# Optimization experiments

Hardware: AMD Instinct MI355X
Metric: run time of the kernel (lower is better)

## Reference

```python
import jax, jax.numpy as jnp
import numpy as np

B, N_REL, N_OBJ, N_ATT, VOCAB, D = 32, 1024, 1024, 4, 2048, 512


def setup_inputs() -> dict:
    key = jax.random.key(0)
    ks = jax.random.split(key, 12)
    inp = {}
    inp["ssg_rel"] = jax.random.randint(ks[0], (B, N_REL, 3), 0, N_OBJ, dtype=jnp.int32)
    inp["ssg_obj"] = jax.random.randint(ks[1], (B, N_OBJ), 0, VOCAB, dtype=jnp.int32)
    inp["ssg_att"] = jax.random.randint(ks[2], (B, N_OBJ, N_ATT), 0, VOCAB, dtype=jnp.int32)
    inp["emb_table"] = jax.random.normal(ks[3], (VOCAB, D), jnp.float32) * 0.02
    def lin(k, fan_in):
        return jax.random.normal(k, (fan_in, D), jnp.float32) * (1.0 / np.sqrt(fan_in))
    inp["W_sbj"] = lin(ks[4], 3 * D); inp["b_sbj"] = jnp.zeros((D,), jnp.float32)
    inp["W_obj"] = lin(ks[5], 3 * D); inp["b_obj"] = jnp.zeros((D,), jnp.float32)
    inp["W_rel"] = lin(ks[6], 3 * D); inp["b_rel"] = jnp.zeros((D,), jnp.float32)
    inp["W_o"] = lin(ks[7], D);      inp["b_o"] = jnp.zeros((D,), jnp.float32)
    inp["W_a"] = lin(ks[8], 2 * D);  inp["b_a"] = jnp.zeros((D,), jnp.float32)
    return inp


def reference(ssg_rel, ssg_obj, ssg_att, emb_table,
              W_sbj, b_sbj, W_obj, b_obj, W_rel, b_rel, W_o, b_o, W_a, b_a):
    # Dropout is identity in eval mode.
    Bq, N_rel, _ = ssg_rel.shape
    _, N_obj, N_att = ssg_att.shape
    d = emb_table.shape[1]

    rel_mask = (ssg_rel[:, :, 2] == 1)[..., None]      # [B, N_rel, 1], True = pad
    obj_mask = ssg_obj == 1                            # [B, N_obj]
    attr_mask = ssg_att == 1                           # [B, N_obj, N_att]

    rel_emb = emb_table[ssg_rel[:, :, 2]]              # [B, N_rel, d]
    obj_emb = emb_table[ssg_obj]                       # [B, N_obj, d]
    attr_emb = emb_table[ssg_att]                      # [B, N_obj, N_att, d]

    sbj_id = ssg_rel[:, :, 0]
    obj_id = ssg_rel[:, :, 1]
    gather = lambda ids: jnp.take_along_axis(obj_emb, ids[..., None], axis=1)  # [B,N_rel,d]
    sbj_g = gather(sbj_id)
    obj_g = gather(obj_id)

    zfill = lambda x: jnp.where(rel_mask, 0.0, x)
    # Sequential overwriting matches the original: rel_obj/rel_rel use the UPDATED sbj/obj feats.
    sbj_f = zfill(jax.nn.relu(jnp.concatenate([sbj_g, obj_g, rel_emb], -1) @ W_sbj + b_sbj))
    obj_f = zfill(jax.nn.relu(jnp.concatenate([sbj_f, obj_g, rel_emb], -1) @ W_obj + b_obj))
    rel_f = zfill(jax.nn.relu(jnp.concatenate([sbj_f, obj_f, rel_emb], -1) @ W_rel + b_rel))

    node = jnp.where(obj_mask[..., None], 0.0, jax.nn.relu(obj_emb @ W_o + b_o))  # [B,N_obj,d]

    att_in = jnp.concatenate(
        [jnp.broadcast_to(obj_emb[:, :, None, :], (Bq, N_obj, N_att, d)), attr_emb], -1)
    att_f = jnp.where(attr_mask[..., None], 0.0, jax.nn.relu(att_in @ W_a + b_a))  # [B,N_obj,N_att,d]

    bidx = jnp.arange(Bq)[:, None]
    node = node.at[bidx, sbj_id].add(sbj_f)
    node = node.at[bidx, obj_id].add(obj_f)

    # Original builds counts=ones(B, 2*N_rel, N_obj+1) then scatters 1s into it -> a no-op,
    # so counts.sum(dim=1) == 2*N_rel everywhere; the divisor is the constant 2*N_rel.
    rel_object_feat = node / jnp.asarray(2.0 * N_rel, node.dtype)

    att_sum = att_f.sum(axis=2)                        # [B, N_obj, d]
    att_cnt = jnp.sum(~attr_mask, axis=-1)             # [B, N_obj] number of valid attrs
    attr_zero = att_cnt == 0
    denom = jnp.maximum(att_cnt, 1).astype(att_sum.dtype)[..., None]
    att_feat = jnp.where(attr_zero[..., None], 0.0, att_sum / denom)

    ssg_feat = jnp.concatenate([rel_object_feat, rel_f, att_feat], axis=1)
    ssg_mask = jnp.concatenate([obj_mask, rel_mask[..., 0], attr_zero], axis=1)[:, None, None, :]
    return ssg_feat, ssg_mask
```

## Files before the change

kernel.cpp:

```cpp
#include <hip/hip_runtime.h>
#include <hip/hip_bf16.h>

typedef __attribute__((ext_vector_type(8))) short bf16x8;
typedef __attribute__((ext_vector_type(4))) float f32x4;

#define N_OBJ 1024
#define N_REL 1024
#define NB 32
#define D 512
#define VOCAB 2048
#define M_ROWS (NB * N_REL)
#define PRE_BLK (VOCAB * D)
#define WT_BLK (D * D)
#define LCAP 64

__device__ __forceinline__ ushort f2bf(float f) {
    union { float f; unsigned u; } v; v.f = f;
    unsigned u = v.u;
    unsigned r = (u + 0x7FFFu + ((u >> 16) & 1u)) >> 16;
    return (ushort)r;
}
__device__ __forceinline__ float bf2f(ushort h) {
    union { unsigned u; float f; } v; v.u = ((unsigned)h) << 16;
    return v.f;
}

__device__ __forceinline__ void gload16(const ushort* g, const ushort* l) {
    __builtin_amdgcn_global_load_lds(
        (const __attribute__((address_space(1))) void*)(unsigned long long)(const void*)g,
        (__attribute__((address_space(3))) void*)(unsigned)(unsigned long long)(const void*)l,
        16, 0, 0);
}
__device__ __forceinline__ unsigned lds_off(const void* p) {
    return (unsigned)(unsigned long long)(const __attribute__((address_space(3))) void*)p;
}
__device__ __forceinline__ bf16x8 ds_read128(unsigned off) {
    bf16x8 r;
    asm volatile("ds_read_b128 %0, %1" : "=v"(r) : "v"(off));
    return r;
}

template <int MODE>
__device__ __forceinline__ void gemm8_body(
    int mt, int nt, int q, int tid, ushort* lds,
    const ushort* __restrict__ A, const ushort* __restrict__ WT,
    ushort* __restrict__ PREB,
    const int* __restrict__ ssg_rel, const int* __restrict__ ssg_obj,
    const float* __restrict__ bias,
    ushort* __restrict__ featbuf, float* __restrict__ out0,
    float* __restrict__ out1) {
    constexpr int KTOT = (MODE == 2) ? 1024 : 512;
    constexpr int NK = KTOT / 32;
    constexpr int LDA = (MODE == 0) ? 512 : 1024;

    const int m0 = mt * 256, n0 = nt * 256;

    const ushort* BT0;
    const ushort* BT1 = nullptr;
    ushort* PREq = nullptr;
    if (MODE == 0) {
        const int wtq[9] = {0, 1, 2, 4, 5, 8, 9, 10, 11};
        BT0 = WT + (size_t)wtq[q] * WT_BLK + (size_t)n0 * 512;
        PREq = PREB + (size_t)q * PRE_BLK;
    } else if (MODE == 1) {
        BT0 = WT + (size_t)3 * WT_BLK + (size_t)n0 * 512;
    } else {
        BT0 = WT + (size_t)6 * WT_BLK + (size_t)n0 * 512;
        BT1 = WT + (size_t)7 * WT_BLK + (size_t)n0 * 512;
    }

    const ushort* Ag = A + (size_t)m0 * LDA;
    const int srow = tid >> 2;
    const int scol = (tid & 3) * 8;

    const int wave = tid >> 6, lane = tid & 63;
    const int wm = wave >> 2, wn = wave & 3;
    const int lr = lane & 15, lk = lane >> 4;

    f32x4 acc[8][4];
#pragma unroll
    for (int mi = 0; mi < 8; mi++)
#pragma unroll
        for (int ni = 0; ni < 4; ni++)
            acc[mi][ni] = (f32x4){0.f, 0.f, 0.f, 0.f};

#define STAGE(KT) do {                                                          \
        int _b = (KT) & 3;                                                      \
        ushort* _dA = &lds[(_b * 2 + 0) * 8192];                                \
        ushort* _dB = &lds[(_b * 2 + 1) * 8192];                                \
        int _k0 = (KT) * 32;                                                    \
        const ushort* _Bb = (MODE == 2 && _k0 >= 512) ? (BT1 + (_k0 - 512))     \
                                                      : (BT0 + _k0);            \
        gload16(Ag + (size_t)(srow) * LDA + _k0 + scol, _dA + srow * 32 + scol);        \
        gload16(Ag + (size_t)(srow + 128) * LDA + _k0 + scol, _dA + (srow + 128) * 32 + scol); \
        gload16(_Bb + (size_t)(srow) * 512 + scol, _dB + srow * 32 + scol);             \
        gload16(_Bb + (size_t)(srow + 128) * 512 + scol, _dB + (srow + 128) * 32 + scol); \
    } while (0)

    STAGE(0); STAGE(1); STAGE(2);

    for (int kt = 0; kt < NK; ++kt) {
        if (kt + 3 < NK) {
            asm volatile("s_waitcnt vmcnt(8)\n\ts_barrier" ::: "memory");
            STAGE(kt + 3);
        } else if (kt + 3 == NK) {
            asm volatile("s_waitcnt vmcnt(8)\n\ts_barrier" ::: "memory");
        } else if (kt + 2 == NK) {
            asm volatile("s_waitcnt vmcnt(4)\n\ts_barrier" ::: "memory");
        } else {
            asm volatile("s_waitcnt vmcnt(0)\n\ts_barrier" ::: "memory");
        }
        {
            int buf = kt & 3;
            unsigned baseA = lds_off(&lds[(buf * 2 + 0) * 8192]) + (unsigned)(wm * 128) * 64 + lk * 16;
            unsigned baseB = lds_off(&lds[(buf * 2 + 1) * 8192]) + (unsigned)(wn * 64) * 64 + lk * 16;
            bf16x8 bfr[4], af[8];
#pragma unroll
            for (int ni = 0; ni < 4; ni++)
                bfr[ni] = ds_read128(baseB + (unsigned)(ni * 16 + lr) * 64);
#pragma unroll
            for (int mi = 0; mi < 8; mi++)
                af[mi] = ds_read128(baseA + (unsigned)(mi * 16 + lr) * 64);
            asm volatile("s_waitcnt lgkmcnt(4)" ::: "memory");
            __builtin_amdgcn_sched_barrier(0);
            __builtin_amdgcn_s_setprio(1);
#pragma unroll
            for (int mi = 0; mi < 4; mi++)
#pragma unroll
                for (int ni = 0; ni < 4; ni++)
                    acc[mi][ni] = __builtin_amdgcn_mfma_f32_16x16x32_bf16(af[mi], bfr[ni], acc[mi][ni], 0, 0, 0);
            __builtin_amdgcn_s_setprio(0);
            asm volatile("s_waitcnt lgkmcnt(0)" ::: "memory");
            __builtin_amdgcn_sched_barrier(0);
            __builtin_amdgcn_s_setprio(1);
#pragma unroll
            for (int mi = 4; mi < 8; mi++)
#pragma unroll
                for (int ni = 0; ni < 4; ni++)
                    acc[mi][ni] = __builtin_amdgcn_mfma_f32_16x16x32_bf16(af[mi], bfr[ni], acc[mi][ni], 0, 0, 0);
            __builtin_amdgcn_s_setprio(0);
        }
    }
#undef STAGE

    if (MODE == 0) {
#pragma unroll
        for (int mi = 0; mi < 8; mi++)
#pragma unroll
            for (int ni = 0; ni < 4; ni++) {
                int ch = n0 + wn * 64 + ni * 16 + lr;
#pragma unroll
                for (int j = 0; j < 4; j++) {
                    int R = m0 + wm * 128 + mi * 16 + lk * 4 + j;
                    PREq[(size_t)R * 512 + ch] = f2bf(acc[mi][ni][j]);
                }
            }
        return;
    }

    __syncthreads();
    int* sIo  = (int*)lds;
    int* sRid = sIo + 256;
    if (tid < 256) {
        int R = m0 + tid;
        int rid = ssg_rel[R * 3 + 2];
        sRid[tid] = rid;
        if (MODE == 1) sIo[tid] = ssg_obj[(R & ~(N_OBJ - 1)) + ssg_rel[R * 3 + 1]];
        if (MODE == 2 && nt == 0) {
            int b = R >> 10, rr = R & (N_REL - 1);
            out1[(size_t)b * 3072 + 1024 + rr] = (rid == 1) ? 1.0f : 0.0f;
        }
    }
    __syncthreads();

#pragma unroll
    for (int mi = 0; mi < 8; mi++) {
#pragma unroll
        for (int ni = 0; ni < 4; ni++) {
            int ch = n0 + wn * 64 + ni * 16 + lr;
#pragma unroll
            for (int j = 0; j < 4; j++) {
                int rl = wm * 128 + mi * 16 + lk * 4 + j;
                int R = m0 + rl;
                float v = acc[mi][ni][j];
                if (MODE == 1) {
                    int rid = sRid[rl];
                    int io = sIo[rl];
                    float t = v + bf2f(PREB[(size_t)3 * PRE_BLK + (size_t)io * 512 + ch])
                                + bf2f(PREB[(size_t)4 * PRE_BLK + (size_t)rid * 512 + ch])
                                + bias[ch];
                    t = fmaxf(t, 0.f);
                    if (rid == 1) t = 0.f;
                    featbuf[(size_t)R * 1024 + 512 + ch] = f2bf(t);
                } else {
                    int rid = sRid[rl];
                    float t = v + bf2f(PREB[(size_t)5 * PRE_BLK + (size_t)rid * 512 + ch])
                                + bias[ch];
                    t = fmaxf(t, 0.f);
                    if (rid == 1) t = 0.f;
                    int b = R >> 10, rr = R & (N_REL - 1);
                    out0[((size_t)(b * 3072 + 1024 + rr)) * 512 + ch] = t;
                }
            }
        }
    }
}

__global__ __launch_bounds__(256)
void k_setup(const float* __restrict__ E, ushort* __restrict__ EB,
             const float* __restrict__ Wsbj, const float* __restrict__ Wobj,
             const float* __restrict__ Wrel, const float* __restrict__ Wo,
             const float* __restrict__ Wa, ushort* __restrict__ WT,
             int* __restrict__ cnt) {
    int blk = blockIdx.x, tid = threadIdx.x;
    if (blk < 1024) {
        int i = blk * 256 + tid;
        float4 v = ((const float4*)E)[i];
        ushort4 o; o.x = f2bf(v.x); o.y = f2bf(v.y); o.z = f2bf(v.z); o.w = f2bf(v.w);
        ((ushort4*)EB)[i] = o;
    } else if (blk < 4096) {
        __shared__ float s[32][33];
        int bb = blk - 1024;
        int q = bb >> 8, rem = bb & 255;
        int bx = rem & 15, by = rem >> 4;
        const float* src; int ro;
        if (q < 3)       { src = Wsbj; ro = q * 512; }
        else if (q < 6)  { src = Wobj; ro = (q - 3) * 512; }
        else if (q < 9)  { src = Wrel; ro = (q - 6) * 512; }
        else if (q == 9) { src = Wo;   ro = 0; }
        else             { src = Wa;   ro = (q - 10) * 512; }
        int tx = tid & 31, ty = tid >> 5;
        int kbase = by * 32, nbase = bx * 32;
#pragma unroll
        for (int i = 0; i < 4; i++) {
            int k = kbase + ty + i * 8;
            s[ty + i * 8][tx] = src[(size_t)(ro + k) * 512 + nbase + tx];
        }
        __syncthreads();
        ushort* dst = WT + (size_t)q * WT_BLK;
#pragma unroll
        for (int i = 0; i < 4; i++) {
            int n = nbase + ty + i * 8;
            dst[(size_t)n * 512 + kbase + tx] = f2bf(s[tx][ty + i * 8]);
        }
    } else {
        cnt[(blk - 4096) * 256 + tid] = 0;
    }
}

__global__ __launch_bounds__(512, 2)
void k_pre_fill(const ushort* __restrict__ EB, const ushort* __restrict__ WT,
                ushort* __restrict__ PREB, const int* __restrict__ ssg_rel,
                int* __restrict__ cnt, int* __restrict__ lists) {
    __shared__ __attribute__((aligned(16))) ushort lds[4 * 2 * 256 * 32];
    int blk = blockIdx.x, tid = threadIdx.x;
    if (blk < 120) {
        int q, mt, nt;
        if (blk < 96) {
            const int qf[6] = {0, 1, 3, 6, 7, 8};
            q = qf[blk >> 4]; mt = (blk & 15) >> 1; nt = blk & 1;
        } else {
            const int qh[3] = {2, 4, 5};
            int b = blk - 96;
            q = qh[b >> 3]; mt = (b & 7) >> 1; nt = b & 1;
        }
        gemm8_body<0>(mt, nt, q, tid, lds, EB, WT, PREB,
                      nullptr, nullptr, nullptr, nullptr, nullptr, nullptr);
    } else {
        int r = (blk - 120) * 512 + tid;
        int bb = r & ~(N_OBJ - 1);
        int sid = ssg_rel[r * 3 + 0];
        int oid = ssg_rel[r * 3 + 1];
        int s0 = atomicAdd(&cnt[bb + sid], 1);
        if (s0 < LCAP) lists[(size_t)(bb + sid) * LCAP + s0] = r * 2;
        int s1 = atomicAdd(&cnt[bb + oid], 1);
        if (s1 < LCAP) lists[(size_t)(bb + oid) * LCAP + s1] = r * 2 + 1;
    }
}

__global__ void k_sbj_att(const int* __restrict__ ssg_rel, const int* __restrict__ ssg_obj,
                          const int* __restrict__ ssg_att,
                          const ushort* __restrict__ PREB,
                          const float* __restrict__ b_sbj, const float* __restrict__ b_a,
                          ushort* __restrict__ featbuf,
                          float* __restrict__ out0, float* __restrict__ out1) {
    int blk = blockIdx.x, tid = threadIdx.x;
    if (blk < 16384) {
        int R = blk * 2 + (tid >> 7);
        int c4 = tid & 127;
        int sid = ssg_rel[R * 3 + 0];
        int oid = ssg_rel[R * 3 + 1];
        int rid = ssg_rel[R * 3 + 2];
        int bb = R & ~(N_OBJ - 1);
        int is_ = ssg_obj[bb + sid];
        int io  = ssg_obj[bb + oid];
        ushort4 p1 = ((const ushort4*)(PREB + (size_t)is_ * 512))[c4];
        ushort4 p2 = ((const ushort4*)(PREB + (size_t)1 * PRE_BLK + (size_t)io * 512))[c4];
        ushort4 p3 = ((const ushort4*)(PREB + (size_t)2 * PRE_BLK + (size_t)rid * 512))[c4];
        float4 b  = ((const float4*)b_sbj)[c4];
        float4 v;
        v.x = fmaxf(bf2f(p1.x) + bf2f(p2.x) + bf2f(p3.x) + b.x, 0.f);
        v.y = fmaxf(bf2f(p1.y) + bf2f(p2.y) + bf2f(p3.y) + b.y, 0.f);
        v.z = fmaxf(bf2f(p1.z) + bf2f(p2.z) + bf2f(p3.z) + b.z, 0.f);
        v.w = fmaxf(bf2f(p1.w) + bf2f(p2.w) + bf2f(p3.w) + b.w, 0.f);
        if (rid == 1) { v.x = v.y = v.z = v.w = 0.f; }
        ushort4 o; o.x = f2bf(v.x); o.y = f2bf(v.y); o.z = f2bf(v.z); o.w = f2bf(v.w);
        *(ushort4*)&featbuf[(size_t)R * 1024 + c4 * 4] = o;
    } else {
        int Ro = (blk - 16384) * 2 + (tid >> 7);
        int c4 = tid & 127;
        int iv = ssg_obj[Ro];
        int bq = Ro >> 10, o = Ro & (N_OBJ - 1);
        int4 jj = ((const int4*)ssg_att)[Ro];
        int j0 = jj.x, j1 = jj.y, j2 = jj.z, j3 = jj.w;
        float4 ba4 = ((const float4*)b_a)[c4];
        ushort4 q7 = ((const ushort4*)(PREB + (size_t)7 * PRE_BLK + (size_t)iv * 512))[c4];
        float bx = bf2f(q7.x) + ba4.x, by = bf2f(q7.y) + ba4.y;
        float bz = bf2f(q7.z) + ba4.z, bw = bf2f(q7.w) + ba4.w;
        int cnt = (j0 != 1) + (j1 != 1) + (j2 != 1) + (j3 != 1);
        float inv = cnt ? 1.0f / (float)cnt : 0.f;
        float sx = 0.f, sy = 0.f, sz = 0.f, sw = 0.f;
        const ushort* A2 = PREB + (size_t)8 * PRE_BLK;
#define ACC_ATT(J) if ((J) != 1) { \
            ushort4 a2 = ((const ushort4*)(A2 + (size_t)(J) * 512))[c4]; \
            sx += fmaxf(bx + bf2f(a2.x), 0.f); sy += fmaxf(by + bf2f(a2.y), 0.f); \
            sz += fmaxf(bz + bf2f(a2.z), 0.f); sw += fmaxf(bw + bf2f(a2.w), 0.f); }
        ACC_ATT(j0) ACC_ATT(j1) ACC_ATT(j2) ACC_ATT(j3)
#undef ACC_ATT
        float4 sv; sv.x = sx * inv; sv.y = sy * inv; sv.z = sz * inv; sv.w = sw * inv;
        ((float4*)out0)[((size_t)(bq * 3072 + 2048 + o)) * 128 + c4] = sv;
        if (c4 == 0) {
            out1[(size_t)bq * 3072 + o] = (iv == 1) ? 1.0f : 0.0f;
            out1[(size_t)bq * 3072 + 2048 + o] = (cnt == 0) ? 1.0f : 0.0f;
        }
    }
}

template <int MODE>
__global__ __launch_bounds__(512, 2)
void k_gemm8(const ushort* __restrict__ A, const ushort* __restrict__ WT,
             ushort* __restrict__ PREB,
             const int* __restrict__ ssg_rel, const int* __restrict__ ssg_obj,
             const float* __restrict__ bias,
             ushort* __restrict__ featbuf, float* __restrict__ out0,
             float* __restrict__ out1) {
    __shared__ __attribute__((aligned(16))) ushort lds[4 * 2 * 256 * 32];
    int x = blockIdx.x & 7, jj = blockIdx.x >> 3;
    int mt = x * 16 + (jj >> 1), nt = jj & 1;
    gemm8_body<MODE>(mt, nt, 0, threadIdx.x, lds, A, WT, PREB,
                     ssg_rel, ssg_obj, bias, featbuf, out0, out1);
}

__global__ void k_nodepass(const int* __restrict__ ssg_obj,
                           const int* __restrict__ cnt, const int* __restrict__ lists,
                           const ushort* __restrict__ feat, const ushort* __restrict__ PREB,
                           const float* __restrict__ b_o, float* __restrict__ out0) {
    int Ro = blockIdx.x * 2 + (threadIdx.x >> 7);
    int c4 = threadIdx.x & 127;
    int iv = ssg_obj[Ro];
    int bq = Ro >> 10, o = Ro & (N_OBJ - 1);

    float4 bo4 = ((const float4*)b_o)[c4];
    ushort4 q6 = ((const ushort4*)(PREB + (size_t)6 * PRE_BLK + (size_t)iv * 512))[c4];
    float a0 = 0.f, a1 = 0.f, a2 = 0.f, a3 = 0.f;
    if (iv != 1) {
        a0 = fmaxf(bf2f(q6.x) + bo4.x, 0.f);
        a1 = fmaxf(bf2f(q6.y) + bo4.y, 0.f);
        a2 = fmaxf(bf2f(q6.z) + bo4.z, 0.f);
        a3 = fmaxf(bf2f(q6.w) + bo4.w, 0.f);
    }
    int e = cnt[Ro]; if (e > LCAP) e = LCAP;
    const int* lst = lists + (size_t)Ro * LCAP;
    for (int i = 0; i < e; ++i) {
        int ent = lst[i];
        ushort4 u = ((const ushort4*)(feat + (size_t)(ent >> 1) * 1024 + (ent & 1) * 512))[c4];
        a0 += bf2f(u.x); a1 += bf2f(u.y); a2 += bf2f(u.z); a3 += bf2f(u.w);
    }
    float4 r;
    r.x = a0 * (1.0f / 2048.0f); r.y = a1 * (1.0f / 2048.0f);
    r.z = a2 * (1.0f / 2048.0f); r.w = a3 * (1.0f / 2048.0f);
    ((float4*)out0)[((size_t)(bq * 3072 + o)) * 128 + c4] = r;
}

extern "C" void kernel_launch(void* const* d_in, const int* in_sizes, int n_in,
                              void* d_out, int out_size, void* d_ws, size_t ws_size,
                              hipStream_t stream) {
    const int*   ssg_rel = (const int*)d_in[0];
    const int*   ssg_obj = (const int*)d_in[1];
    const int*   ssg_att = (const int*)d_in[2];
    const float* emb     = (const float*)d_in[3];
    const float* Wsbj    = (const float*)d_in[4];
    const float* bsbj    = (const float*)d_in[5];
    const float* Wobj    = (const float*)d_in[6];
    const float* bobj    = (const float*)d_in[7];
    const float* Wrel    = (const float*)d_in[8];
    const float* brel    = (const float*)d_in[9];
    const float* Wo      = (const float*)d_in[10];
    const float* bo      = (const float*)d_in[11];
    const float* Wa      = (const float*)d_in[12];
    const float* ba      = (const float*)d_in[13];

    float* out0 = (float*)d_out;
    float* out1 = out0 + (size_t)NB * 3072 * 512;

    char* w = (char*)d_ws;
    ushort* EB     = (ushort*)w; w += (size_t)VOCAB * D * 2;
    ushort* WT     = (ushort*)w; w += (size_t)12 * WT_BLK * 2;
    ushort* PREB   = (ushort*)w; w += (size_t)9 * PRE_BLK * 2;
    ushort* feat   = (ushort*)w; w += (size_t)M_ROWS * 1024 * 2;
    int*    cnt    = (int*)   w; w += (size_t)32768 * 4;
    int*    lists  = (int*)   w; w += (size_t)32768 * LCAP * 4;

    k_setup<<<dim3(4224), dim3(256), 0, stream>>>(emb, EB, Wsbj, Wobj, Wrel, Wo, Wa, WT, cnt);
    k_pre_fill<<<dim3(184), dim3(512), 0, stream>>>(EB, WT, PREB, ssg_rel, cnt, lists);
    k_sbj_att<<<dim3(32768), dim3(256), 0, stream>>>(ssg_rel, ssg_obj, ssg_att, PREB,
                                                     bsbj, ba, feat, out0, out1);
    k_gemm8<1><<<dim3(256), dim3(512), 0, stream>>>(feat, WT, PREB, ssg_rel, ssg_obj,
                                                    bobj, feat, nullptr, nullptr);
    k_gemm8<2><<<dim3(256), dim3(512), 0, stream>>>(feat, WT, PREB, ssg_rel, ssg_obj,
                                                    brel, nullptr, out0, out1);
    k_nodepass<<<dim3(M_ROWS / 2), dim3(256), 0, stream>>>(ssg_obj, cnt, lists,
                                                           feat, PREB, bo, out0);
}
```

Before: 191.6 us.

## Fuse node aggregation into rel GEMM tail and merge sbj/att threads

Removes the separate node-pass kernel. Each block of the MODE-2 GEMM now loops over 128 object rows after its tile work, summing the gathered sbj/obj features into the node output. The sbj and attribute branches of k_sbj_att now run in the same thread, which halves the grid. This saves a kernel launch and some block scheduling overhead. The cost is that the gather-heavy node aggregation now runs serially on only 256 blocks, adding to the GEMM's critical path.

Measured after the change: 226.4 us. 18.2% more time.

```diff
diff --git a/kernel.cpp b/kernel.cpp
--- a/kernel.cpp
+++ b/kernel.cpp
@@ -285,9 +285,11 @@
                           ushort* __restrict__ featbuf,
                           float* __restrict__ out0, float* __restrict__ out1) {
     int blk = blockIdx.x, tid = threadIdx.x;
-    if (blk < 16384) {
-        int R = blk * 2 + (tid >> 7);
-        int c4 = tid & 127;
+    int idx = blk * 2 + (tid >> 7);
+    int c4 = tid & 127;
+
+    {
+        int R = idx;
         int sid = ssg_rel[R * 3 + 0];
         int oid = ssg_rel[R * 3 + 1];
         int rid = ssg_rel[R * 3 + 2];
@@ -306,9 +308,10 @@
         if (rid == 1) { v.x = v.y = v.z = v.w = 0.f; }
         ushort4 o; o.x = f2bf(v.x); o.y = f2bf(v.y); o.z = f2bf(v.z); o.w = f2bf(v.w);
         *(ushort4*)&featbuf[(size_t)R * 1024 + c4 * 4] = o;
-    } else {
-        int Ro = (blk - 16384) * 2 + (tid >> 7);
-        int c4 = tid & 127;
+    }
+
+    {
+        int Ro = idx;
         int iv = ssg_obj[Ro];
         int bq = Ro >> 10, o = Ro & (N_OBJ - 1);
         int4 jj = ((const int4*)ssg_att)[Ro];
@@ -343,43 +346,46 @@
              const int* __restrict__ ssg_rel, const int* __restrict__ ssg_obj,
              const float* __restrict__ bias,
              ushort* __restrict__ featbuf, float* __restrict__ out0,
-             float* __restrict__ out1) {
+             float* __restrict__ out1,
+             const int* __restrict__ ncnt, const int* __restrict__ lists,
+             const float* __restrict__ b_o) {
     __shared__ __attribute__((aligned(16))) ushort lds[4 * 2 * 256 * 32];
     int x = blockIdx.x & 7, jj = blockIdx.x >> 3;
     int mt = x * 16 + (jj >> 1), nt = jj & 1;
     gemm8_body<MODE>(mt, nt, 0, threadIdx.x, lds, A, WT, PREB,
                      ssg_rel, ssg_obj, bias, featbuf, out0, out1);
-}
-
-__global__ void k_nodepass(const int* __restrict__ ssg_obj,
-                           const int* __restrict__ cnt, const int* __restrict__ lists,
-                           const ushort* __restrict__ feat, const ushort* __restrict__ PREB,
-                           const float* __restrict__ b_o, float* __restrict__ out0) {
-    int Ro = blockIdx.x * 2 + (threadIdx.x >> 7);
-    int c4 = threadIdx.x & 127;
-    int iv = ssg_obj[Ro];
-    int bq = Ro >> 10, o = Ro & (N_OBJ - 1);
-
-    float4 bo4 = ((const float4*)b_o)[c4];
-    ushort4 q6 = ((const ushort4*)(PREB + (size_t)6 * PRE_BLK + (size_t)iv * 512))[c4];
-    float a0 = 0.f, a1 = 0.f, a2 = 0.f, a3 = 0.f;
-    if (iv != 1) {
-        a0 = fmaxf(bf2f(q6.x) + bo4.x, 0.f);
-        a1 = fmaxf(bf2f(q6.y) + bo4.y, 0.f);
-        a2 = fmaxf(bf2f(q6.z) + bo4.z, 0.f);
-        a3 = fmaxf(bf2f(q6.w) + bo4.w, 0.f);
-    }
-    int e = cnt[Ro]; if (e > LCAP) e = LCAP;
-    const int* lst = lists + (size_t)Ro * LCAP;
-    for (int i = 0; i < e; ++i) {
-        int ent = lst[i];
-        ushort4 u = ((const ushort4*)(feat + (size_t)(ent >> 1) * 1024 + (ent & 1) * 512))[c4];
-        a0 += bf2f(u.x); a1 += bf2f(u.y); a2 += bf2f(u.z); a3 += bf2f(u.w);
-    }
-    float4 r;
-    r.x = a0 * (1.0f / 2048.0f); r.y = a1 * (1.0f / 2048.0f);
-    r.z = a2 * (1.0f / 2048.0f); r.w = a3 * (1.0f / 2048.0f);
-    ((float4*)out0)[((size_t)(bq * 3072 + o)) * 128 + c4] = r;
+
+    if (MODE == 2) {
+        int bid = blockIdx.x;
+        int c4 = threadIdx.x & 127;
+        int sub = threadIdx.x >> 7;
+        const float4 bo4 = ((const float4*)b_o)[c4];
+#pragma unroll 1
+        for (int i = 0; i < 32; ++i) {
+            int Ro = bid * 128 + i * 4 + sub;
+            int iv = ssg_obj[Ro];
+            int bq = Ro >> 10, o = Ro & (N_OBJ - 1);
+            ushort4 q6 = ((const ushort4*)(PREB + (size_t)6 * PRE_BLK + (size_t)iv * 512))[c4];
+            float a0 = 0.f, a1 = 0.f, a2 = 0.f, a3 = 0.f;
+            if (iv != 1) {
+                a0 = fmaxf(bf2f(q6.x) + bo4.x, 0.f);
+                a1 = fmaxf(bf2f(q6.y) + bo4.y, 0.f);
+                a2 = fmaxf(bf2f(q6.z) + bo4.z, 0.f);
+                a3 = fmaxf(bf2f(q6.w) + bo4.w, 0.f);
+            }
+            int e = ncnt[Ro]; if (e > LCAP) e = LCAP;
+            const int* lst = lists + (size_t)Ro * LCAP;
+            for (int t = 0; t < e; ++t) {
+                int ent = lst[t];
+                ushort4 u = ((const ushort4*)(featbuf + (size_t)(ent >> 1) * 1024 + (ent & 1) * 512))[c4];
+                a0 += bf2f(u.x); a1 += bf2f(u.y); a2 += bf2f(u.z); a3 += bf2f(u.w);
+            }
+            float4 r;
+            r.x = a0 * (1.0f / 2048.0f); r.y = a1 * (1.0f / 2048.0f);
+            r.z = a2 * (1.0f / 2048.0f); r.w = a3 * (1.0f / 2048.0f);
+            ((float4*)out0)[((size_t)(bq * 3072 + o)) * 128 + c4] = r;
+        }
+    }
 }
 
 extern "C" void kernel_launch(void* const* d_in, const int* in_sizes, int n_in,
@@ -413,12 +419,12 @@
 
     k_setup<<<dim3(4224), dim3(256), 0, stream>>>(emb, EB, Wsbj, Wobj, Wrel, Wo, Wa, WT, cnt);
     k_pre_fill<<<dim3(184), dim3(512), 0, stream>>>(EB, WT, PREB, ssg_rel, cnt, lists);
-    k_sbj_att<<<dim3(32768), dim3(256), 0, stream>>>(ssg_rel, ssg_obj, ssg_att, PREB,
+    k_sbj_att<<<dim3(16384), dim3(256), 0, stream>>>(ssg_rel, ssg_obj, ssg_att, PREB,
                                                      bsbj, ba, feat, out0, out1);
     k_gemm8<1><<<dim3(256), dim3(512), 0, stream>>>(feat, WT, PREB, ssg_rel, ssg_obj,
-                                                    bobj, feat, nullptr, nullptr);
+                                                    bobj, feat, nullptr, nullptr,
+                                                    nullptr, nullptr, nullptr);
     k_gemm8<2><<<dim3(256), dim3(512), 0, stream>>>(feat, WT, PREB, ssg_rel, ssg_obj,
-                                                    brel, nullptr, out0, out1);
-    k_nodepass<<<dim3(M_ROWS / 2), dim3(256), 0, stream>>>(ssg_obj, cnt, lists,
-                                                           feat, PREB, bo, out0);
-}
+                                                    brel, feat, out0, out1,
+                                                    cnt, lists, bo);
+}
```
